# Kernel optimization log

Hardware: AMD Instinct MI355X
Metric: run time of the kernel (lower is better)

## Reference

```python
import jax, jax.numpy as jnp
import numpy as np

N_TOKENS = 32768
D_MODEL = 1024


def setup_inputs() -> dict:
    key = jax.random.key(0)
    kx, kr, kw1, kb1, kw2, kb2 = jax.random.split(key, 6)
    scale = 1.0 / np.sqrt(D_MODEL)
    x = jax.random.normal(kx, (N_TOKENS, D_MODEL), dtype=jnp.float32)
    # RandomScatterRouter: each token independently routed to one of 2 experts
    route = jax.random.randint(kr, (N_TOKENS,), 0, 2, dtype=jnp.int32)
    W1 = jax.random.normal(kw1, (D_MODEL, D_MODEL), dtype=jnp.float32) * scale
    b1 = jax.random.normal(kb1, (D_MODEL,), dtype=jnp.float32) * scale
    W2 = jax.random.normal(kw2, (D_MODEL, D_MODEL), dtype=jnp.float32) * scale
    b2 = jax.random.normal(kb2, (D_MODEL,), dtype=jnp.float32) * scale
    return {"x": x, "W1": W1, "b1": b1, "W2": W2, "b2": b2, "route": route}


def reference(x, W1, b1, W2, b2, route):
    # Semantics of scatter -> expert linears -> gather(reverse_indice):
    #   out[i] = x[i] @ W_{route[i]} + b_{route[i]}  (original token order restored)
    # jit-friendly form: mask-partition tokens to each expert (m0 + m1 == 1),
    # run the two expert GEMMs on the disjoint partitions, sum to recombine.
    m0 = (route == 0).astype(x.dtype)[:, None]  # [N, 1]
    m1 = 1.0 - m0
    y0 = (x * m0) @ W1 + b1 * m0  # expert-1 output on its tokens, zeros elsewhere
    y1 = (x * m1) @ W2 + b2 * m1  # expert-2 output on its tokens, zeros elsewhere
    return y0 + y1
```

## Files before the change

### kernel.cpp

```cpp
#include <hip/hip_runtime.h>

#define NT 32768
#define DM 1024
#define NTOT (NT + 128)
#define NKT (DM / 64)

typedef __bf16 bf16x8 __attribute__((ext_vector_type(8)));
typedef __bf16 bf16x4 __attribute__((ext_vector_type(4)));
typedef float f32x4 __attribute__((ext_vector_type(4)));

#define GLD16(g, l)                                                            \
  __builtin_amdgcn_global_load_lds(                                            \
      (const __attribute__((address_space(1))) void*)(g),                      \
      (__attribute__((address_space(3))) void*)(l), 16, 0, 0)

__device__ __forceinline__ unsigned short f2bf(float f) {
  unsigned u = __float_as_uint(f);
  u += 0x7fffu + ((u >> 16) & 1u);
  return (unsigned short)(u >> 16);
}

__global__ void wt_k(const float* __restrict__ W1, const float* __restrict__ W2,
                     unsigned short* __restrict__ Wt) {
  const float* __restrict__ W = blockIdx.z ? W2 : W1;
  unsigned short* __restrict__ dst = Wt + (size_t)blockIdx.z * DM * DM;
  __shared__ float tile[32][33];
  int tx = threadIdx.x, ty = threadIdx.y;
  int n0 = blockIdx.x * 32, k0 = blockIdx.y * 32;
#pragma unroll
  for (int i = 0; i < 32; i += 8)
    tile[ty + i][tx] = W[(size_t)(k0 + ty + i) * DM + n0 + tx];
  __syncthreads();
#pragma unroll
  for (int i = 0; i < 32; i += 8)
    dst[(size_t)(n0 + ty + i) * DM + k0 + tx] = f2bf(tile[tx][ty + i]);
}

__global__ __launch_bounds__(1024) void route_k(const int* __restrict__ route,
                                                int* __restrict__ idx,
                                                int* __restrict__ counters) {
  __shared__ int wsum[16];
  const int t = threadIdx.x;
  const int lane = t & 63, wv = t >> 6;
  const int base = t * 32;
  const int4* rp = (const int4*)(route + base);
  unsigned mask = 0;
#pragma unroll
  for (int v = 0; v < 8; ++v) {
    int4 q = rp[v];
    mask |= (unsigned)(q.x == 0) << (v * 4 + 0);
    mask |= (unsigned)(q.y == 0) << (v * 4 + 1);
    mask |= (unsigned)(q.z == 0) << (v * 4 + 2);
    mask |= (unsigned)(q.w == 0) << (v * 4 + 3);
  }
  const int c0 = __popc(mask);
  int s = c0;
#pragma unroll
  for (int d = 1; d < 64; d <<= 1) {
    int v = __shfl_up(s, (unsigned)d, 64);
    if (lane >= d) s += v;
  }
  if (lane == 63) wsum[wv] = s;
  __syncthreads();
  int waveBase = 0, total0 = 0;
#pragma unroll
  for (int w = 0; w < 16; ++w) {
    int v = wsum[w];
    if (w < wv) waveBase += v;
    total0 += v;
  }
  const int ex0 = waveBase + s - c0;
  int slot0 = ex0;
  int slot1 = NTOT - 1 - (base - ex0);
#pragma unroll
  for (int i = 0; i < 32; ++i) {
    int token = base + i;
    if ((mask >> i) & 1) idx[slot0++] = token;
    else                 idx[slot1--] = token;
  }
  if (t == 0) { counters[0] = total0; counters[1] = NT - total0; }
}

__global__ __launch_bounds__(256, 3) void gemm_k(
    const float* __restrict__ x,
    const unsigned short* __restrict__ Wt,
    const float* __restrict__ b1, const float* __restrict__ b2,
    const int* __restrict__ idx, const int* __restrict__ counters,
    float* __restrict__ out) {
  __shared__ unsigned short As[128 * 64];
  __shared__ unsigned short Bs[2][128 * 64];

  const int t = threadIdx.x;
  const int lane = t & 63, wave = t >> 6;

  const int lin = blockIdx.y * 8 + blockIdx.x;
  const int L = (lin & 7) * 257 + (lin >> 3);
  const int row0 = (L >> 3) * 128;
  const int col0 = (L & 7) * 128;

  const int n0 = counters[0];
  const int expert = (row0 < n0) ? 0 : 1;
  const unsigned short* Wte = Wt + (size_t)expert * DM * DM;
  const float* bias = expert ? b2 : b1;

  const int wr = (wave >> 1) * 64;
  const int wc = (wave & 1) * 64;
  const int lr = lane & 15;

  const int rsub = t >> 4;
  const int c16 = t & 15;
  const float* rowp[8];
#pragma unroll
  for (int p = 0; p < 8; ++p) {
    int gr = row0 + p * 16 + rsub;
    int tok = idx[gr];
    if (gr >= n0 && gr < n0 + 128) tok = 0;
    rowp[p] = x + (size_t)tok * DM;
  }

  float4 a[8];
  f32x4 acc[4][4] = {};

#define LOADA(k0)                                                              \
  _Pragma("unroll") for (int p = 0; p < 8; ++p)                                \
      a[p] = *(const float4*)(rowp[p] + (k0) + c16 * 4);

#define WRITEA()                                                               \
  _Pragma("unroll") for (int p = 0; p < 8; ++p) {                              \
    int r = p * 16 + rsub;                                                     \
    int off = (r * 8 + ((c16 >> 1) ^ (r & 7))) * 16 + (c16 & 1) * 8;           \
    bf16x4 pk;                                                                 \
    pk[0] = (__bf16)a[p].x; pk[1] = (__bf16)a[p].y;                            \
    pk[2] = (__bf16)a[p].z; pk[3] = (__bf16)a[p].w;                            \
    *(bf16x4*)((char*)&As[0] + off) = pk;                                      \
  }

#define STAGEB(k0, bufw)                                                       \
  _Pragma("unroll") for (int p = 0; p < 4; ++p) {                              \
    int q = p * 256 + t;                                                       \
    int r = q >> 3;                                                            \
    int c = ((q & 7) ^ (r & 7)) * 8;                                           \
    GLD16(Wte + (size_t)(col0 + r) * DM + (k0) + c, &Bs[bufw][q * 8]);         \
  }

  LOADA(0);
  STAGEB(0, 0);

#pragma unroll 2
  for (int kt = 0; kt < NKT; ++kt) {
    const int buf = kt & 1;
    WRITEA();
    __syncthreads();
    if (kt < NKT - 1) {
      LOADA((kt + 1) * 64);
      STAGEB((kt + 1) * 64, buf ^ 1);
    }
#pragma unroll
    for (int s = 0; s < 2; ++s) {
      const int cb = s * 4 + (lane >> 4);
      bf16x8 af[4], bfr[4];
#pragma unroll
      for (int i = 0; i < 4; ++i) {
        int r = wr + i * 16 + lr;
        af[i] = *(const bf16x8*)&As[(r * 8 + (cb ^ (r & 7))) * 8];
      }
#pragma unroll
      for (int j = 0; j < 4; ++j) {
        int r = wc + j * 16 + lr;
        bfr[j] = *(const bf16x8*)&Bs[buf][(r * 8 + (cb ^ (r & 7))) * 8];
      }
#pragma unroll
      for (int i = 0; i < 4; ++i)
#pragma unroll
        for (int j = 0; j < 4; ++j)
          acc[i][j] = __builtin_amdgcn_mfma_f32_16x16x32_bf16(af[i], bfr[j], acc[i][j], 0, 0, 0);
    }
    asm volatile("s_waitcnt lgkmcnt(0)" ::: "memory");
    __builtin_amdgcn_sched_barrier(0);
    __builtin_amdgcn_s_barrier();
    __builtin_amdgcn_sched_barrier(0);
  }

#pragma unroll
  for (int i = 0; i < 4; ++i) {
#pragma unroll
    for (int reg = 0; reg < 4; ++reg) {
      int gr = row0 + wr + i * 16 + (lane >> 4) * 4 + reg;
      if (gr < n0 || gr >= n0 + 128) {
        int dest = idx[gr];
#pragma unroll
        for (int j = 0; j < 4; ++j) {
          int gc = col0 + wc + j * 16 + (lane & 15);
          out[(size_t)dest * DM + gc] = acc[i][j][reg] + bias[gc];
        }
      }
    }
  }
#undef LOADA
#undef WRITEA
#undef STAGEB
}

extern "C" void kernel_launch(void* const* d_in, const int* in_sizes, int n_in,
                              void* d_out, int out_size, void* d_ws, size_t ws_size,
                              hipStream_t stream) {
  const float* x   = (const float*)d_in[0];
  const float* W1  = (const float*)d_in[1];
  const float* b1  = (const float*)d_in[2];
  const float* W2  = (const float*)d_in[3];
  const float* b2  = (const float*)d_in[4];
  const int*   route = (const int*)d_in[5];
  float* out = (float*)d_out;

  char* ws = (char*)d_ws;
  unsigned short* Wt = (unsigned short*)ws;
  size_t off = (size_t)2 * DM * DM * 2;
  int* idx = (int*)(ws + off);
  int* counters = idx + NTOT;

  route_k<<<1, 1024, 0, stream>>>(route, idx, counters);
  wt_k<<<dim3(DM / 32, DM / 32, 2), dim3(32, 8), 0, stream>>>(W1, W2, Wt);
  gemm_k<<<dim3(8, NTOT / 128), 256, 0, stream>>>(x, Wt, b1, b2, idx, counters, out);
}
```

Measured before the change: 395.2 us.

## Double-buffer A tile in LDS and prefetch activations two tiles ahead

The A (activation) tile gets its own LDS double buffer, and a register set prefetches x two k-tiles ahead. The fp32-to-bf16 conversion and LDS write for the next tile now happen after the MFMAs, with a single barrier per iteration. Explicit vmcnt waits replace the __syncthreads. This is meant to hide global load latency of the gathered activations behind compute, at the cost of doubled A LDS and registers, with occupancy hint lowered from 3 to 2 blocks per CU.

```diff
diff --git a/kernel.cpp b/kernel.cpp
--- a/kernel.cpp
+++ b/kernel.cpp
@@ -81,13 +81,13 @@
   if (t == 0) { counters[0] = total0; counters[1] = NT - total0; }
 }
 
-__global__ __launch_bounds__(256, 3) void gemm_k(
+__global__ __launch_bounds__(256, 2) void gemm_k(
     const float* __restrict__ x,
     const unsigned short* __restrict__ Wt,
     const float* __restrict__ b1, const float* __restrict__ b2,
     const int* __restrict__ idx, const int* __restrict__ counters,
     float* __restrict__ out) {
-  __shared__ unsigned short As[128 * 64];
+  __shared__ unsigned short As[2][128 * 64];
   __shared__ unsigned short Bs[2][128 * 64];
 
   const int t = threadIdx.x;
@@ -118,21 +118,21 @@
     rowp[p] = x + (size_t)tok * DM;
   }
 
-  float4 a[8];
+  float4 a[2][8];
   f32x4 acc[4][4] = {};
 
-#define LOADA(k0)                                                              \
+#define LOADA(k0, s)                                                           \
   _Pragma("unroll") for (int p = 0; p < 8; ++p)                                \
-      a[p] = *(const float4*)(rowp[p] + (k0) + c16 * 4);
-
-#define WRITEA()                                                               \
+      a[s][p] = *(const float4*)(rowp[p] + (k0) + c16 * 4);
+
+#define WRITEA(s, bufw)                                                        \
   _Pragma("unroll") for (int p = 0; p < 8; ++p) {                              \
     int r = p * 16 + rsub;                                                     \
     int off = (r * 8 + ((c16 >> 1) ^ (r & 7))) * 16 + (c16 & 1) * 8;           \
     bf16x4 pk;                                                                 \
-    pk[0] = (__bf16)a[p].x; pk[1] = (__bf16)a[p].y;                            \
-    pk[2] = (__bf16)a[p].z; pk[3] = (__bf16)a[p].w;                            \
-    *(bf16x4*)((char*)&As[0] + off) = pk;                                      \
+    pk[0] = (__bf16)a[s][p].x; pk[1] = (__bf16)a[s][p].y;                      \
+    pk[2] = (__bf16)a[s][p].z; pk[3] = (__bf16)a[s][p].w;                      \
+    *(bf16x4*)((char*)&As[bufw][0] + off) = pk;                                \
   }
 
 #define STAGEB(k0, bufw)                                                       \
@@ -143,18 +143,20 @@
     GLD16(Wte + (size_t)(col0 + r) * DM + (k0) + c, &Bs[bufw][q * 8]);         \
   }
 
-  LOADA(0);
+  LOADA(0, 0);
   STAGEB(0, 0);
-
-#pragma unroll 2
+  WRITEA(0, 0);
+  LOADA(64, 1);
+  asm volatile("s_waitcnt vmcnt(8) lgkmcnt(0)" ::: "memory");
+  __builtin_amdgcn_sched_barrier(0);
+  __builtin_amdgcn_s_barrier();
+  __builtin_amdgcn_sched_barrier(0);
+
+#pragma unroll
   for (int kt = 0; kt < NKT; ++kt) {
     const int buf = kt & 1;
-    WRITEA();
-    __syncthreads();
-    if (kt < NKT - 1) {
-      LOADA((kt + 1) * 64);
-      STAGEB((kt + 1) * 64, buf ^ 1);
-    }
+    if (kt < NKT - 1) STAGEB((kt + 1) * 64, buf ^ 1);
+    if (kt < NKT - 2) LOADA((kt + 2) * 64, buf);
 #pragma unroll
     for (int s = 0; s < 2; ++s) {
       const int cb = s * 4 + (lane >> 4);
@@ -162,7 +164,7 @@
 #pragma unroll
       for (int i = 0; i < 4; ++i) {
         int r = wr + i * 16 + lr;
-        af[i] = *(const bf16x8*)&As[(r * 8 + (cb ^ (r & 7))) * 8];
+        af[i] = *(const bf16x8*)&As[buf][(r * 8 + (cb ^ (r & 7))) * 8];
       }
 #pragma unroll
       for (int j = 0; j < 4; ++j) {
@@ -175,10 +177,16 @@
         for (int j = 0; j < 4; ++j)
           acc[i][j] = __builtin_amdgcn_mfma_f32_16x16x32_bf16(af[i], bfr[j], acc[i][j], 0, 0, 0);
     }
-    asm volatile("s_waitcnt lgkmcnt(0)" ::: "memory");
-    __builtin_amdgcn_sched_barrier(0);
-    __builtin_amdgcn_s_barrier();
-    __builtin_amdgcn_sched_barrier(0);
+    if (kt < NKT - 1) {
+      WRITEA(buf ^ 1, buf ^ 1);
+      if (kt <= NKT - 3)
+        asm volatile("s_waitcnt vmcnt(8) lgkmcnt(0)" ::: "memory");
+      else
+        asm volatile("s_waitcnt vmcnt(0) lgkmcnt(0)" ::: "memory");
+      __builtin_amdgcn_sched_barrier(0);
+      __builtin_amdgcn_s_barrier();
+      __builtin_amdgcn_sched_barrier(0);
+    }
   }
 
 #pragma unroll
```

Result: faster. 375.8 us (-4.9%).

## Pre-gather and convert tokens to bf16 buffer, stream A via global_load_lds

Applied to the files above, without the earlier changes.

A new copy kernel gathers the routed token rows of x into an expert-sorted bf16 workspace buffer. The GEMM then stages A straight from that buffer with direct global-to-LDS loads, the same way it stages B. This removes the per-tile fp32 loads, conversion and LDS writes done in registers inside the GEMM, and halves the bytes read for A across the column blocks. In exchange it adds an extra pass over x and a 64MB workspace. It also drops B double buffering for a simpler single-buffer loop with occupancy raised to 4 blocks, so overlap now relies on concurrent blocks rather than in-block prefetch.

```diff
diff --git a/kernel.cpp b/kernel.cpp
--- a/kernel.cpp
+++ b/kernel.cpp
@@ -3,10 +3,8 @@
 #define NT 32768
 #define DM 1024
 #define NTOT (NT + 128)
-#define NKT (DM / 64)
 
 typedef __bf16 bf16x8 __attribute__((ext_vector_type(8)));
-typedef __bf16 bf16x4 __attribute__((ext_vector_type(4)));
 typedef float f32x4 __attribute__((ext_vector_type(4)));
 
 #define GLD16(g, l)                                                            \
@@ -81,14 +79,41 @@
   if (t == 0) { counters[0] = total0; counters[1] = NT - total0; }
 }
 
-__global__ __launch_bounds__(256, 3) void gemm_k(
-    const float* __restrict__ x,
+__global__ __launch_bounds__(256) void copy_k(const float* __restrict__ x,
+                                              const int* __restrict__ idx,
+                                              const int* __restrict__ counters,
+                                              unsigned short* __restrict__ xp) {
+  const int t = threadIdx.x, lane = t & 63, wave = t >> 6;
+  const int slot0 = blockIdx.x * 64;
+  const int n0 = counters[0];
+  for (int row = wave; row < 64; row += 4) {
+    int slot = slot0 + row;
+    if (slot >= n0 && slot < n0 + 128) continue;
+    int tok = idx[slot];
+    const float4* src = (const float4*)(x + (size_t)tok * DM);
+    bf16x8* dst = (bf16x8*)(xp + (size_t)slot * DM);
+#pragma unroll
+    for (int p = 0; p < 2; ++p) {
+      float4 v0 = src[p * 128 + lane * 2];
+      float4 v1 = src[p * 128 + lane * 2 + 1];
+      bf16x8 pk;
+      pk[0] = (__bf16)v0.x; pk[1] = (__bf16)v0.y;
+      pk[2] = (__bf16)v0.z; pk[3] = (__bf16)v0.w;
+      pk[4] = (__bf16)v1.x; pk[5] = (__bf16)v1.y;
+      pk[6] = (__bf16)v1.z; pk[7] = (__bf16)v1.w;
+      dst[p * 64 + lane] = pk;
+    }
+  }
+}
+
+__global__ __launch_bounds__(256, 4) void gemm_k(
+    const unsigned short* __restrict__ xp,
     const unsigned short* __restrict__ Wt,
     const float* __restrict__ b1, const float* __restrict__ b2,
     const int* __restrict__ idx, const int* __restrict__ counters,
     float* __restrict__ out) {
   __shared__ unsigned short As[128 * 64];
-  __shared__ unsigned short Bs[2][128 * 64];
+  __shared__ unsigned short Bs[128 * 64];
 
   const int t = threadIdx.x;
   const int lane = t & 63, wave = t >> 6;
@@ -107,54 +132,18 @@
   const int wc = (wave & 1) * 64;
   const int lr = lane & 15;
 
-  const int rsub = t >> 4;
-  const int c16 = t & 15;
-  const float* rowp[8];
-#pragma unroll
-  for (int p = 0; p < 8; ++p) {
-    int gr = row0 + p * 16 + rsub;
-    int tok = idx[gr];
-    if (gr >= n0 && gr < n0 + 128) tok = 0;
-    rowp[p] = x + (size_t)tok * DM;
-  }
-
-  float4 a[8];
   f32x4 acc[4][4] = {};
 
-#define LOADA(k0)                                                              \
-  _Pragma("unroll") for (int p = 0; p < 8; ++p)                                \
-      a[p] = *(const float4*)(rowp[p] + (k0) + c16 * 4);
-
-#define WRITEA()                                                               \
-  _Pragma("unroll") for (int p = 0; p < 8; ++p) {                              \
-    int r = p * 16 + rsub;                                                     \
-    int off = (r * 8 + ((c16 >> 1) ^ (r & 7))) * 16 + (c16 & 1) * 8;           \
-    bf16x4 pk;                                                                 \
-    pk[0] = (__bf16)a[p].x; pk[1] = (__bf16)a[p].y;                            \
-    pk[2] = (__bf16)a[p].z; pk[3] = (__bf16)a[p].w;                            \
-    *(bf16x4*)((char*)&As[0] + off) = pk;                                      \
-  }
-
-#define STAGEB(k0, bufw)                                                       \
-  _Pragma("unroll") for (int p = 0; p < 4; ++p) {                              \
-    int q = p * 256 + t;                                                       \
-    int r = q >> 3;                                                            \
-    int c = ((q & 7) ^ (r & 7)) * 8;                                           \
-    GLD16(Wte + (size_t)(col0 + r) * DM + (k0) + c, &Bs[bufw][q * 8]);         \
-  }
-
-  LOADA(0);
-  STAGEB(0, 0);
-
-#pragma unroll 2
-  for (int kt = 0; kt < NKT; ++kt) {
-    const int buf = kt & 1;
-    WRITEA();
+  for (int k0 = 0; k0 < DM; k0 += 64) {
+#pragma unroll
+    for (int p = 0; p < 4; ++p) {
+      int q = p * 256 + t;
+      int r = q >> 3;
+      int c = ((q & 7) ^ (r & 7)) * 8;
+      GLD16(xp  + (size_t)(row0 + r) * DM + k0 + c, As + q * 8);
+      GLD16(Wte + (size_t)(col0 + r) * DM + k0 + c, Bs + q * 8);
+    }
     __syncthreads();
-    if (kt < NKT - 1) {
-      LOADA((kt + 1) * 64);
-      STAGEB((kt + 1) * 64, buf ^ 1);
-    }
 #pragma unroll
     for (int s = 0; s < 2; ++s) {
       const int cb = s * 4 + (lane >> 4);
@@ -167,7 +156,7 @@
 #pragma unroll
       for (int j = 0; j < 4; ++j) {
         int r = wc + j * 16 + lr;
-        bfr[j] = *(const bf16x8*)&Bs[buf][(r * 8 + (cb ^ (r & 7))) * 8];
+        bfr[j] = *(const bf16x8*)&Bs[(r * 8 + (cb ^ (r & 7))) * 8];
       }
 #pragma unroll
       for (int i = 0; i < 4; ++i)
@@ -175,10 +164,7 @@
         for (int j = 0; j < 4; ++j)
           acc[i][j] = __builtin_amdgcn_mfma_f32_16x16x32_bf16(af[i], bfr[j], acc[i][j], 0, 0, 0);
     }
-    asm volatile("s_waitcnt lgkmcnt(0)" ::: "memory");
-    __builtin_amdgcn_sched_barrier(0);
-    __builtin_amdgcn_s_barrier();
-    __builtin_amdgcn_sched_barrier(0);
+    __syncthreads();
   }
 
 #pragma unroll
@@ -196,9 +182,6 @@
       }
     }
   }
-#undef LOADA
-#undef WRITEA
-#undef STAGEB
 }
 
 extern "C" void kernel_launch(void* const* d_in, const int* in_sizes, int n_in,
@@ -213,12 +196,15 @@
   float* out = (float*)d_out;
 
   char* ws = (char*)d_ws;
-  unsigned short* Wt = (unsigned short*)ws;
-  size_t off = (size_t)2 * DM * DM * 2;
+  unsigned short* xp = (unsigned short*)ws;
+  size_t off = (size_t)NTOT * DM * 2;
+  unsigned short* Wt = (unsigned short*)(ws + off);
+  off += (size_t)2 * DM * DM * 2;
   int* idx = (int*)(ws + off);
   int* counters = idx + NTOT;
 
   route_k<<<1, 1024, 0, stream>>>(route, idx, counters);
+  copy_k<<<NTOT / 64, 256, 0, stream>>>(x, idx, counters, xp);
   wt_k<<<dim3(DM / 32, DM / 32, 2), dim3(32, 8), 0, stream>>>(W1, W2, Wt);
-  gemm_k<<<dim3(8, NTOT / 128), 256, 0, stream>>>(x, Wt, b1, b2, idx, counters, out);
-}
+  gemm_k<<<dim3(8, NTOT / 128), 256, 0, stream>>>(xp, Wt, b1, b2, idx, counters, out);
+}
```

New measurement: 350.8 us. 11.2% less time.
